# Kernel tuning notes

Measured on AMD Instinct MI355X. Metric: run time of the kernel, lower is better.

Reference implementation:

```python
import jax, jax.numpy as jnp
from jax import lax
import numpy as np

B, T, I, H, L, O = 256, 512, 1, 256, 4, 1


def setup_inputs() -> dict:
    key = jax.random.key(0)
    ks = jax.random.split(key, 4 * L + 3)
    s = 1.0 / np.sqrt(H)
    inp = {"x": jax.random.normal(ks[0], (B, T, I), dtype=jnp.float32)}
    for l in range(L):
        in_dim = I if l == 0 else H
        inp[f"W_ih{l}"] = jax.random.uniform(ks[1 + 4 * l], (4 * H, in_dim), minval=-s, maxval=s, dtype=jnp.float32)
        inp[f"W_hh{l}"] = jax.random.uniform(ks[2 + 4 * l], (4 * H, H), minval=-s, maxval=s, dtype=jnp.float32)
        inp[f"b_ih{l}"] = jax.random.uniform(ks[3 + 4 * l], (4 * H,), minval=-s, maxval=s, dtype=jnp.float32)
        inp[f"b_hh{l}"] = jax.random.uniform(ks[4 + 4 * l], (4 * H,), minval=-s, maxval=s, dtype=jnp.float32)
    inp["fc_W"] = jax.random.uniform(ks[-2], (O, H), minval=-s, maxval=s, dtype=jnp.float32)
    inp["fc_b"] = jax.random.uniform(ks[-1], (O,), minval=-s, maxval=s, dtype=jnp.float32)
    return inp


def _lstm_layer(x_seq, W_ih, W_hh, b_ih, b_hh):
    # x_seq: [B, T, in_dim] -> hidden sequence [B, T, H]
    b, t = x_seq.shape[0], x_seq.shape[1]
    h = W_hh.shape[1]
    # precompute input projections for all timesteps: [T, B, 4H]
    xg = jnp.einsum('bti,gi->tbg', x_seq, W_ih) + b_ih + b_hh

    def step(carry, xg_t):
        hp, cp = carry
        gates = xg_t + hp @ W_hh.T  # [B, 4H]
        i, f, g, o = jnp.split(gates, 4, axis=-1)  # PyTorch gate order: i,f,g,o
        i = jax.nn.sigmoid(i)
        f = jax.nn.sigmoid(f)
        g = jnp.tanh(g)
        o = jax.nn.sigmoid(o)
        c = f * cp + i * g
        hn = o * jnp.tanh(c)
        return (hn, c), hn

    h0 = jnp.zeros((b, h), x_seq.dtype)
    _, hs = lax.scan(step, (h0, h0), xg)
    return jnp.transpose(hs, (1, 0, 2))  # [B, T, H]


def reference(x, W_ih0, W_hh0, b_ih0, b_hh0, W_ih1, W_hh1, b_ih1, b_hh1,
              W_ih2, W_hh2, b_ih2, b_hh2, W_ih3, W_hh3, b_ih3, b_hh3, fc_W, fc_b):
    layers = [(W_ih0, W_hh0, b_ih0, b_hh0), (W_ih1, W_hh1, b_ih1, b_hh1),
              (W_ih2, W_hh2, b_ih2, b_hh2), (W_ih3, W_hh3, b_ih3, b_hh3)]
    out = x
    for Wi, Wh, bi, bh in layers:
        out = _lstm_layer(out, Wi, Wh, bi, bh)
    # final linear on last timestep hidden: [B, H] -> [B, O]
    return out[:, -1, :] @ fc_W.T + fc_b
```

## Files before the change

### kernel.cpp

```cpp
#include <hip/hip_runtime.h>
#include <stdint.h>

#define T_ 512
#define H_ 256
#define MB 32
#define NBUF 8
#define ISLOT 8192
#define NWG 256

typedef __attribute__((ext_vector_type(8))) short  short8;
typedef __attribute__((ext_vector_type(4))) float  floatx4;
typedef __attribute__((ext_vector_type(4))) unsigned int uint4v;
typedef unsigned long long ull;

struct Params {
  const float* x;
  const float* Wih[4]; const float* Whh[4]; const float* bih[4]; const float* bhh[4];
  const float* fcW; const float* fcb;
  int*   flags;
  int*   xcd;
  short* hring;
};

__device__ __forceinline__ short f2bf(float f){
  uint32_t u = __builtin_bit_cast(uint32_t, f);
  u += 0x7fffu + ((u >> 16) & 1u);
  return (short)(u >> 16);
}
__device__ __forceinline__ float bf2f(short s){
  uint32_t u = ((uint32_t)(uint16_t)s) << 16;
  return __builtin_bit_cast(float, u);
}
__device__ __forceinline__ float sigm(float v){ return 1.0f / (1.0f + __expf(-v)); }
__device__ __forceinline__ float tanh_(float v){
  float a = fabsf(v);
  float e = __expf(-2.0f * a);
  float r = (1.0f - e) / (1.0f + e);
  return v < 0.0f ? -r : r;
}

__device__ __forceinline__ void a_st32(unsigned* p, unsigned v){
  __hip_atomic_store(p, v, __ATOMIC_RELAXED, __HIP_MEMORY_SCOPE_AGENT);
}
__device__ __forceinline__ int a_ldi(const int* p){
  return __hip_atomic_load(p, __ATOMIC_RELAXED, __HIP_MEMORY_SCOPE_AGENT);
}
__device__ __forceinline__ void a_sti(int* p, int v){
  __hip_atomic_store(p, v, __ATOMIC_RELAXED, __HIP_MEMORY_SCOPE_AGENT);
}

__device__ __forceinline__ int ctr_poll(const int* p){
  int v; int z = 0;
  asm volatile("global_atomic_add %0, %1, %2, off sc0\n\t"
               "s_waitcnt vmcnt(0)"
               : "=v"(v) : "v"(p), "v"(z) : "memory");
  return v;
}
__device__ __forceinline__ void ctr_post(int* p){
  int one = 1;
  asm volatile("global_atomic_add %0, %1, off" :: "v"(p), "v"(one) : "memory");
}

template<bool SL> __device__ __forceinline__ void ld16t(uint4v& d, const void* p){
  if constexpr (SL) asm volatile("global_load_dwordx4 %0, %1, off sc0 sc1" : "=v"(d) : "v"(p));
  else              asm volatile("global_load_dwordx4 %0, %1, off sc0"     : "=v"(d) : "v"(p));
}
template<bool SL> __device__ __forceinline__ void st32t(unsigned* p, unsigned v){
  if constexpr (SL) a_st32(p, v);
  else asm volatile("global_store_dword %0, %1, off sc0" :: "v"(p), "v"(v) : "memory");
}
typedef __attribute__((address_space(1))) const void as1void;
typedef __attribute__((address_space(3))) void       as3void;
__device__ __forceinline__ void gld_lds16(const void* g, void* l){
  __builtin_amdgcn_global_load_lds((as1void*)g, (as3void*)l, 16, 0, 1);
}
__device__ __forceinline__ void inv_l1(){
  asm volatile("buffer_inv sc0" ::: "memory");
}

__device__ __forceinline__ void ldf32(float& d, const void* p){
  asm volatile("global_load_dword %0, %1, off" : "=v"(d) : "v"(p));
}
template<int N> __device__ __forceinline__ void waitvm(){
  if constexpr (N == 0) asm volatile("s_waitcnt vmcnt(0)" ::: "memory");
  else if constexpr (N == 1) asm volatile("s_waitcnt vmcnt(1)" ::: "memory");
  else                       asm volatile("s_waitcnt vmcnt(4)" ::: "memory");
}
__device__ __forceinline__ void bar_lds(){
  asm volatile("s_waitcnt lgkmcnt(0)" ::: "memory");
  __builtin_amdgcn_s_barrier();
}
__device__ __forceinline__ void bar_only(){
  __builtin_amdgcn_s_barrier();
}

#define MFMA(a,b,c) __builtin_amdgcn_mfma_f32_16x16x32_bf16((a),(b),(c),0,0,0)

__device__ __forceinline__ void wpoll(const int* p, int thr, bool& dead){
  if (dead) return;
  int guard = 0;
  for (;;){
    int v = a_ldi(p);
    if (__all((int)(v >= thr))) break;
    if (++guard > (1 << 16)) { dead = true; break; }
  }
}

__device__ __forceinline__ void cpoll(const int* self, const int* up, const int* down,
                                      int t, bool& dead){
  if (dead) return;
  const int lane = threadIdx.x & 63;
  const int* p = nullptr; int thr = 0;
  if (lane == 0)            { p = self; thr = t; }
  else if (lane == 1 && up) { p = up;   thr = t + 2; }
  else if (lane == 2 && down && ((t & 3) == 0)){ p = down; thr = t - 4; }
  if (thr > T_) thr = T_;
  thr <<= 3;
  int guard = 0;
  for (;;){
    int v = p ? ctr_poll(p) : 0x7fffffff;
    if (__all((int)(v >= thr))) break;
    __builtin_amdgcn_s_sleep(1);
    if (++guard > (1 << 14)) { dead = true; break; }
  }
}

template<bool L0, bool SL>
__device__ __forceinline__ void run_cell(const Params& p, int g, int l, int slice,
    short* a_frag, float (*g_lds)[MB][34], float (*bias_lds)[32],
    float (*wih0_lds)[32], float* x0_lds)
{
  constexpr int KBT = L0 ? 8 : 16;
  const int tid = threadIdx.x, lane = tid & 63, wave = tid >> 6;
  const int n15 = lane & 15, q4 = lane >> 4;

  int* fl_self = p.flags + (g * 4 + l) * 32;
  int* fl_up   = L0 ? fl_self : fl_self - 32;
  int* fl_down = (l < 3) ? fl_self + 32 : fl_self;
  short* hr_self = p.hring + (size_t)((g * 4 + l) * NBUF) * ISLOT;
  const short* hr_up = L0 ? (const short*)nullptr
                          : hr_self - (size_t)NBUF * ISLOT;

  int* ctr_self = fl_self;
  const int* ctr_up   = L0 ? (const int*)nullptr : fl_self - 32;
  const int* ctr_down = (l < 3) ? fl_self + 32 : (const int*)nullptr;

  if (tid < 128){
    int gt = tid >> 5, j = tid & 31;
    int gr = gt * 256 + slice * 32 + j;
    bias_lds[gt][j] = p.bih[l][gr] + p.bhh[l][gr];
    if (L0) wih0_lds[gt][j] = p.Wih[0][gr];
  }

  short8 wf0[KBT], wf1[KBT];
  const int g0 = wave * 256 + slice * 32 + n15;
  const int g1 = g0 + 16;
  #pragma unroll
  for (int kb = 0; kb < KBT; ++kb){
    const float* base; int kk;
    if (L0)          { base = p.Whh[0]; kk = kb * 32 + q4 * 8; }
    else if (kb < 8) { base = p.Wih[l]; kk = kb * 32 + q4 * 8; }
    else             { base = p.Whh[l]; kk = (kb - 8) * 32 + q4 * 8; }
    const float* p0 = base + (size_t)g0 * H_ + kk;
    const float* p1 = base + (size_t)g1 * H_ + kk;
    short8 a, b;
    #pragma unroll
    for (int i = 0; i < 8; ++i){ a[i] = f2bf(p0[i]); b[i] = f2bf(p1[i]); }
    wf0[kb] = a; wf1[kb] = b;
  }

  float c00 = 0.f, c01 = 0.f, c10 = 0.f, c11 = 0.f;
  const int r0 = (tid >> 4) * 2, r1 = r0 + 1;
  const int pc = (tid & 15) * 2;

  const int* pp; int dlt;
  if (lane < 8)      { pp = fl_self + lane; dlt = 0; }
  else if (lane < 16){ if (L0){ pp = fl_self; dlt = -1000000; }
                       else   { pp = fl_up + (lane - 8); dlt = 2; } }
  else if (lane < 24){ if (l < 3){ pp = fl_down + (lane - 16); dlt = -7; }
                       else      { pp = fl_self; dlt = -1000000; } }
  else               { pp = fl_self + (lane & 7); dlt = -1000000; }
  bool dead = false;

  uint4v* fragv = (uint4v*)a_frag;
  uint4v px[4];
  float xcur = 0.f;

  if (!L0){
    if constexpr (SL){
      wpoll(fl_up + (lane & 7), 1, dead);
    } else {
      if (wave == 0) cpoll(ctr_self, ctr_up, ctr_down, -1, dead);
      __syncthreads();
      inv_l1();
    }
    const char* s = (const char*)hr_up;
    #pragma unroll
    for (int k = 0; k < 4; ++k) ld16t<SL>(px[k], s + (size_t)(k * 256 + tid) * 16);
  } else if (wave == 0 && lane < MB){
    ldf32(xcur, &p.x[(size_t)(g * MB + lane) * T_]);
  }
  waitvm<0>();
  __syncthreads();

  for (int t = 0; t < T_; ++t){
    const bool havh = (t > 0);
    const bool pf = (t + 1 < T_);
    const int hbase = L0 ? 0 : 1024;
    uint4v hv[4];
    floatx4 acc[2][2][2] = {};

    if constexpr (SL){
      { int thr = t + dlt; if (thr > T_) thr = T_;
        wpoll(pp, thr, dead); }
      if (!L0){
        #pragma unroll
        for (int k = 0; k < 4; ++k) fragv[k * 256 + tid] = px[k];
      } else if (wave == 0 && lane < MB){
        x0_lds[lane] = xcur;
      }
      if (havh){
        const char* s = (const char*)(hr_self + (size_t)((t - 1) & 7) * ISLOT);
        #pragma unroll
        for (int k = 0; k < 4; ++k) ld16t<SL>(hv[k], s + (size_t)(k * 256 + tid) * 16);
      }
      if (!L0){
        if (pf){
          const char* s = (const char*)(hr_up + (size_t)((t + 1) & 7) * ISLOT);
          #pragma unroll
          for (int k = 0; k < 4; ++k) ld16t<SL>(px[k], s + (size_t)(k * 256 + tid) * 16);
        }
      } else if (wave == 0 && lane < MB && pf){
        ldf32(xcur, &p.x[(size_t)(g * MB + lane) * T_ + (t + 1)]);
      }
      bar_lds();
      if (!L0){
        #pragma unroll
        for (int kb = 0; kb < 8; ++kb){
          #pragma unroll
          for (int mt = 0; mt < 2; ++mt){
            short8 af = *(short8*)&a_frag[(kb * 2 + mt) * 512 + lane * 8];
            int pr = kb & 1;
            acc[mt][0][pr] = MFMA(af, wf0[kb], acc[mt][0][pr]);
            acc[mt][1][pr] = MFMA(af, wf1[kb], acc[mt][1][pr]);
          }
        }
      }
      if (!L0){ if (pf) waitvm<4>(); else waitvm<0>(); }
      else    { if (wave == 0 && pf) waitvm<1>(); else waitvm<0>(); }
      if (havh){
        #pragma unroll
        for (int k = 0; k < 4; ++k) fragv[hbase + k * 256 + tid] = hv[k];
      } else {
        uint4v z = {0, 0, 0, 0};
        #pragma unroll
        for (int k = 0; k < 4; ++k) fragv[hbase + k * 256 + tid] = z;
      }
      bar_lds();
    } else if constexpr (!L0){
      #pragma unroll
      for (int k = 0; k < 4; ++k) fragv[k * 256 + tid] = px[k];
      bar_lds();
      #pragma unroll
      for (int kb = 0; kb < 4; ++kb){
        #pragma unroll
        for (int mt = 0; mt < 2; ++mt){
          short8 af = *(short8*)&a_frag[(kb * 2 + mt) * 512 + lane * 8];
          int pr = kb & 1;
          acc[mt][0][pr] = MFMA(af, wf0[kb], acc[mt][0][pr]);
          acc[mt][1][pr] = MFMA(af, wf1[kb], acc[mt][1][pr]);
        }
      }
      if (wave == 0) cpoll(ctr_self, ctr_up, ctr_down, t, dead);
      bar_only();
      inv_l1();
      if (havh){
        const char* s = (const char*)(hr_self + (size_t)((t - 1) & 7) * ISLOT);
        #pragma unroll
        for (int k = 0; k < 4; ++k){
          const char* src = s + (size_t)(k * 256 + tid) * 16;
          gld_lds16(src, (void*)&fragv[hbase + k * 256 + (tid & ~63)]);
        }
      }
      if (pf){
        const char* s = (const char*)(hr_up + (size_t)((t + 1) & 7) * ISLOT);
        #pragma unroll
        for (int k = 0; k < 4; ++k) ld16t<SL>(px[k], s + (size_t)(k * 256 + tid) * 16);
      }
      #pragma unroll
      for (int kb = 4; kb < 8; ++kb){
        #pragma unroll
        for (int mt = 0; mt < 2; ++mt){
          short8 af = *(short8*)&a_frag[(kb * 2 + mt) * 512 + lane * 8];
          int pr = kb & 1;
          acc[mt][0][pr] = MFMA(af, wf0[kb], acc[mt][0][pr]);
          acc[mt][1][pr] = MFMA(af, wf1[kb], acc[mt][1][pr]);
        }
      }
      if (pf) waitvm<4>(); else waitvm<0>();
      if (!havh){
        uint4v z = {0, 0, 0, 0};
        #pragma unroll
        for (int k = 0; k < 4; ++k) fragv[hbase + k * 256 + tid] = z;
      }
      bar_lds();
    } else {
      if (wave == 0) cpoll(ctr_self, ctr_up, ctr_down, t, dead);
      if (wave == 0 && lane < MB) x0_lds[lane] = xcur;
      bar_lds();
      inv_l1();
      if (havh){
        const char* s = (const char*)(hr_self + (size_t)((t - 1) & 7) * ISLOT);
        #pragma unroll
        for (int k = 0; k < 4; ++k){
          const char* src = s + (size_t)(k * 256 + tid) * 16;
          gld_lds16(src, (void*)&fragv[hbase + k * 256 + (tid & ~63)]);
        }
      }
      if (wave == 0 && lane < MB && pf){
        ldf32(xcur, &p.x[(size_t)(g * MB + lane) * T_ + (t + 1)]);
      }
      if (wave == 0 && pf) waitvm<1>(); else waitvm<0>();
      if (!havh){
        uint4v z = {0, 0, 0, 0};
        #pragma unroll
        for (int k = 0; k < 4; ++k) fragv[hbase + k * 256 + tid] = z;
      }
      bar_lds();
    }

    #pragma unroll
    for (int kb = (L0 ? 0 : 8); kb < KBT; ++kb){
      #pragma unroll
      for (int mt = 0; mt < 2; ++mt){
        short8 af = *(short8*)&a_frag[(kb * 2 + mt) * 512 + lane * 8];
        int pr = kb & 1;
        acc[mt][0][pr] = MFMA(af, wf0[kb], acc[mt][0][pr]);
        acc[mt][1][pr] = MFMA(af, wf1[kb], acc[mt][1][pr]);
      }
    }
    #pragma unroll
    for (int mt = 0; mt < 2; ++mt){
      floatx4 s0 = acc[mt][0][0] + acc[mt][0][1];
      floatx4 s1 = acc[mt][1][0] + acc[mt][1][1];
      int mrow = mt * 16 + q4 * 4;
      #pragma unroll
      for (int r = 0; r < 4; ++r){
        g_lds[wave][mrow + r][n15]      = s0[r];
        g_lds[wave][mrow + r][16 + n15] = s1[r];
      }
    }
    bar_lds();

    {
      float xs0 = 0.f, xs1 = 0.f;
      if (L0){ xs0 = x0_lds[r0]; xs1 = x0_lds[r1]; }
      float2 bi = *(const float2*)&bias_lds[0][pc];
      float2 bf = *(const float2*)&bias_lds[1][pc];
      float2 bg = *(const float2*)&bias_lds[2][pc];
      float2 bo = *(const float2*)&bias_lds[3][pc];
      float2 wi = {0.f,0.f}, wf = {0.f,0.f}, wg = {0.f,0.f}, wo = {0.f,0.f};
      if (L0){
        wi = *(const float2*)&wih0_lds[0][pc];
        wf = *(const float2*)&wih0_lds[1][pc];
        wg = *(const float2*)&wih0_lds[2][pc];
        wo = *(const float2*)&wih0_lds[3][pc];
      }
      short* slot = hr_self + (size_t)(t & 7) * ISLOT;
      #pragma unroll
      for (int rr = 0; rr < 2; ++rr){
        const int row = rr ? r1 : r0;
        const float xs = rr ? xs1 : xs0;
        float2 vi = *(const float2*)&g_lds[0][row][pc];
        float2 vf = *(const float2*)&g_lds[1][row][pc];
        float2 vg = *(const float2*)&g_lds[2][row][pc];
        float2 vo = *(const float2*)&g_lds[3][row][pc];
        float gi0 = vi.x + bi.x, gi1 = vi.y + bi.y;
        float gf0 = vf.x + bf.x, gf1 = vf.y + bf.y;
        float gg0 = vg.x + bg.x, gg1 = vg.y + bg.y;
        float go0 = vo.x + bo.x, go1 = vo.y + bo.y;
        if (L0){
          gi0 += xs * wi.x; gi1 += xs * wi.y;
          gf0 += xs * wf.x; gf1 += xs * wf.y;
          gg0 += xs * wg.x; gg1 += xs * wg.y;
          go0 += xs * wo.x; go1 += xs * wo.y;
        }
        float i0 = sigm(gi0), i1 = sigm(gi1);
        float f0 = sigm(gf0), f1 = sigm(gf1);
        float gv0 = tanh_(gg0), gv1 = tanh_(gg1);
        float o0 = sigm(go0), o1 = sigm(go1);
        float& ca = rr ? c10 : c00;
        float& cb = rr ? c11 : c01;
        ca = f0 * ca + i0 * gv0;
        cb = f1 * cb + i1 * gv1;
        float h0 = o0 * tanh_(ca);
        float h1 = o1 * tanh_(cb);
        unsigned pk = (unsigned)(uint16_t)f2bf(h0) | ((unsigned)(uint16_t)f2bf(h1) << 16);
        unsigned off = (unsigned)((slice * 2 + (row >> 4)) * 512
                     + ((pc >> 3) * 16 + (row & 15)) * 8 + (pc & 7));
        st32t<SL>((unsigned*)(slot + off), pk);
      }
    }

    waitvm<0>();
    bar_only();
    if (tid == 0){
      if constexpr (SL) a_sti(fl_self + slice, t + 1);
      else              ctr_post(ctr_self);
    }
  }
}

__global__ __launch_bounds__(256, 1) void lstm_kernel(Params p){
  __shared__ short a_frag[32 * 512];
  __shared__ float g_lds[4][MB][34];
  __shared__ float bias_lds[4][32];
  __shared__ float wih0_lds[4][32];
  __shared__ float x0_lds[MB];
  __shared__ int   fsh;

  const int bid   = blockIdx.x;
  const int g     = bid & 7;
  const int l     = (bid >> 3) & 3;
  const int slice = bid >> 5;

  int xcc;
  asm volatile("s_getreg_b32 %0, hwreg(HW_REG_XCC_ID)" : "=s"(xcc));
  const int me = xcc + 1;
  if (threadIdx.x == 0) a_sti(&p.xcd[bid], me);
  int fast;
  {
    const int lane = threadIdx.x & 63;
    const int idx = lane & 31;
    const int* xp = p.xcd + (idx >> 2) * 32 + (idx & 3) * 8 + g;
    int v = 0, guard = 0; bool giveup = false;
    for (;;){
      v = a_ldi(xp);
      if (__all((int)(v != 0))) break;
      if (++guard > (1 << 22)) { giveup = true; break; }
    }
    fast = (!giveup && __all((int)(v == me))) ? 1 : 0;
  }
  if (threadIdx.x == 0) fsh = 1;
  __syncthreads();
  if (!fast) fsh = 0;
  __syncthreads();
  fast = fsh;

  if (l == 0){
    if (fast) run_cell<true , false>(p, g, 0, slice, a_frag, g_lds, bias_lds, wih0_lds, x0_lds);
    else      run_cell<true , true >(p, g, 0, slice, a_frag, g_lds, bias_lds, wih0_lds, x0_lds);
  } else {
    if (fast) run_cell<false, false>(p, g, l, slice, a_frag, g_lds, bias_lds, wih0_lds, x0_lds);
    else      run_cell<false, true >(p, g, l, slice, a_frag, g_lds, bias_lds, wih0_lds, x0_lds);
  }
}

__global__ void fc_kernel(const short* __restrict__ hring, const float* __restrict__ fcW,
                          const float* __restrict__ fcb, float* __restrict__ out){
  int b = blockIdx.x, lane = threadIdx.x;
  int g = b >> 5, m = b & 31;
  int mt = m >> 4, mm = m & 15;
  const short* base = hring + (size_t)((g * 4 + 3) * NBUF + ((T_ - 1) & 7)) * ISLOT;
  float s = 0.f;
  #pragma unroll
  for (int k = 0; k < 4; ++k){
    int d = lane + 64 * k;
    int kb = d >> 5, koff = d & 31;
    short hv = base[(kb * 2 + mt) * 512 + ((koff >> 3) * 16 + mm) * 8 + (koff & 7)];
    s += bf2f(hv) * fcW[d];
  }
  #pragma unroll
  for (int off = 32; off; off >>= 1) s += __shfl_down(s, off);
  if (lane == 0) out[b] = s + fcb[0];
}

extern "C" void kernel_launch(void* const* d_in, const int* in_sizes, int n_in,
                              void* d_out, int out_size, void* d_ws, size_t ws_size,
                              hipStream_t stream) {
  Params P;
  P.x = (const float*)d_in[0];
  for (int l = 0; l < 4; ++l){
    P.Wih[l] = (const float*)d_in[1 + 4*l];
    P.Whh[l] = (const float*)d_in[2 + 4*l];
    P.bih[l] = (const float*)d_in[3 + 4*l];
    P.bhh[l] = (const float*)d_in[4 + 4*l];
  }
  P.fcW = (const float*)d_in[17];
  P.fcb = (const float*)d_in[18];

  char* ws = (char*)d_ws;
  P.flags = (int*)ws;
  P.xcd   = (int*)(ws + 4096);
  P.hring = (short*)(ws + 16384);

  hipMemsetAsync(ws, 0, 8192, stream);
  hipLaunchKernelGGL(lstm_kernel, dim3(NWG), dim3(256), 0, stream, P);
  hipLaunchKernelGGL(fc_kernel, dim3(256), dim3(64), 0, stream,
                     P.hring, P.fcW, P.fcb, (float*)d_out);
}
```

Baseline: 1.536 ms.

## Post per-wave counter arrivals and drop trailing barrier in counter-sync LSTM path

Restructures the non-flag (counter) synchronisation path so every wave polls the counters and posts its own arrival, instead of wave 0 polling and tid 0 posting after a block barrier. The poll threshold is scaled by 32 instead of 8 to match the per-wave posts. Layer-0 input staging is double-buffered so the next x value is written during the current step. The point is to remove a block-wide barrier and serial poll from each recurrent step, at the cost of more atomic traffic on the counters and more polling lanes.

```diff
diff --git a/kernel.cpp b/kernel.cpp
--- a/kernel.cpp
+++ b/kernel.cpp
@@ -115,7 +115,7 @@
   else if (lane == 1 && up) { p = up;   thr = t + 2; }
   else if (lane == 2 && down && ((t & 3) == 0)){ p = down; thr = t - 4; }
   if (thr > T_) thr = T_;
-  thr <<= 3;
+  thr <<= 5;
   int guard = 0;
   for (;;){
     int v = p ? ctr_poll(p) : 0x7fffffff;
@@ -128,7 +128,7 @@
 template<bool L0, bool SL>
 __device__ __forceinline__ void run_cell(const Params& p, int g, int l, int slice,
     short* a_frag, float (*g_lds)[MB][34], float (*bias_lds)[32],
-    float (*wih0_lds)[32], float* x0_lds)
+    float (*wih0_lds)[32], float (*x0_lds)[MB])
 {
   constexpr int KBT = L0 ? 8 : 16;
   const int tid = threadIdx.x, lane = tid & 63, wave = tid >> 6;
@@ -185,39 +185,95 @@
   uint4v* fragv = (uint4v*)a_frag;
   uint4v px[4];
   float xcur = 0.f;
-
-  if (!L0){
-    if constexpr (SL){
+  const int hbase = L0 ? 0 : 1024;
+
+  auto pointwise = [&](int t){
+    float xs0 = 0.f, xs1 = 0.f;
+    if (L0){ xs0 = x0_lds[t & 1][r0]; xs1 = x0_lds[t & 1][r1]; }
+    float2 bi = *(const float2*)&bias_lds[0][pc];
+    float2 bf = *(const float2*)&bias_lds[1][pc];
+    float2 bg = *(const float2*)&bias_lds[2][pc];
+    float2 bo = *(const float2*)&bias_lds[3][pc];
+    float2 wi = {0.f,0.f}, wf = {0.f,0.f}, wg = {0.f,0.f}, wo = {0.f,0.f};
+    if (L0){
+      wi = *(const float2*)&wih0_lds[0][pc];
+      wf = *(const float2*)&wih0_lds[1][pc];
+      wg = *(const float2*)&wih0_lds[2][pc];
+      wo = *(const float2*)&wih0_lds[3][pc];
+    }
+    short* slot = hr_self + (size_t)(t & 7) * ISLOT;
+    #pragma unroll
+    for (int rr = 0; rr < 2; ++rr){
+      const int row = rr ? r1 : r0;
+      const float xs = rr ? xs1 : xs0;
+      float2 vi = *(const float2*)&g_lds[0][row][pc];
+      float2 vf = *(const float2*)&g_lds[1][row][pc];
+      float2 vg = *(const float2*)&g_lds[2][row][pc];
+      float2 vo = *(const float2*)&g_lds[3][row][pc];
+      float gi0 = vi.x + bi.x, gi1 = vi.y + bi.y;
+      float gf0 = vf.x + bf.x, gf1 = vf.y + bf.y;
+      float gg0 = vg.x + bg.x, gg1 = vg.y + bg.y;
+      float go0 = vo.x + bo.x, go1 = vo.y + bo.y;
+      if (L0){
+        gi0 += xs * wi.x; gi1 += xs * wi.y;
+        gf0 += xs * wf.x; gf1 += xs * wf.y;
+        gg0 += xs * wg.x; gg1 += xs * wg.y;
+        go0 += xs * wo.x; go1 += xs * wo.y;
+      }
+      float i0 = sigm(gi0), i1 = sigm(gi1);
+      float f0 = sigm(gf0), f1 = sigm(gf1);
+      float gv0 = tanh_(gg0), gv1 = tanh_(gg1);
+      float o0 = sigm(go0), o1 = sigm(go1);
+      float& ca = rr ? c10 : c00;
+      float& cb = rr ? c11 : c01;
+      ca = f0 * ca + i0 * gv0;
+      cb = f1 * cb + i1 * gv1;
+      float h0 = o0 * tanh_(ca);
+      float h1 = o1 * tanh_(cb);
+      unsigned pk = (unsigned)(uint16_t)f2bf(h0) | ((unsigned)(uint16_t)f2bf(h1) << 16);
+      unsigned off = (unsigned)((slice * 2 + (row >> 4)) * 512
+                   + ((pc >> 3) * 16 + (row & 15)) * 8 + (pc & 7));
+      st32t<SL>((unsigned*)(slot + off), pk);
+    }
+  };
+  auto gates_out = [&](floatx4 (&acc)[2][2][2]){
+    #pragma unroll
+    for (int mt = 0; mt < 2; ++mt){
+      floatx4 s0 = acc[mt][0][0] + acc[mt][0][1];
+      floatx4 s1 = acc[mt][1][0] + acc[mt][1][1];
+      int mrow = mt * 16 + q4 * 4;
+      #pragma unroll
+      for (int r = 0; r < 4; ++r){
+        g_lds[wave][mrow + r][n15]      = s0[r];
+        g_lds[wave][mrow + r][16 + n15] = s1[r];
+      }
+    }
+  };
+
+  if constexpr (SL){
+    if (!L0){
       wpoll(fl_up + (lane & 7), 1, dead);
-    } else {
-      if (wave == 0) cpoll(ctr_self, ctr_up, ctr_down, -1, dead);
-      __syncthreads();
-      inv_l1();
-    }
-    const char* s = (const char*)hr_up;
-    #pragma unroll
-    for (int k = 0; k < 4; ++k) ld16t<SL>(px[k], s + (size_t)(k * 256 + tid) * 16);
-  } else if (wave == 0 && lane < MB){
-    ldf32(xcur, &p.x[(size_t)(g * MB + lane) * T_]);
-  }
-  waitvm<0>();
-  __syncthreads();
-
-  for (int t = 0; t < T_; ++t){
-    const bool havh = (t > 0);
-    const bool pf = (t + 1 < T_);
-    const int hbase = L0 ? 0 : 1024;
-    uint4v hv[4];
-    floatx4 acc[2][2][2] = {};
-
-    if constexpr (SL){
+      const char* s = (const char*)hr_up;
+      #pragma unroll
+      for (int k = 0; k < 4; ++k) ld16t<SL>(px[k], s + (size_t)(k * 256 + tid) * 16);
+    } else if (wave == 0 && lane < MB){
+      ldf32(xcur, &p.x[(size_t)(g * MB + lane) * T_]);
+    }
+    waitvm<0>();
+    __syncthreads();
+
+    for (int t = 0; t < T_; ++t){
+      const bool havh = (t > 0);
+      const bool pf = (t + 1 < T_);
+      floatx4 acc[2][2][2] = {};
+      uint4v hv[4];
       { int thr = t + dlt; if (thr > T_) thr = T_;
         wpoll(pp, thr, dead); }
       if (!L0){
         #pragma unroll
         for (int k = 0; k < 4; ++k) fragv[k * 256 + tid] = px[k];
       } else if (wave == 0 && lane < MB){
-        x0_lds[lane] = xcur;
+        x0_lds[0][lane] = xcur;
       }
       if (havh){
         const char* s = (const char*)(hr_self + (size_t)((t - 1) & 7) * ISLOT);
@@ -257,12 +313,8 @@
         for (int k = 0; k < 4; ++k) fragv[hbase + k * 256 + tid] = z;
       }
       bar_lds();
-    } else if constexpr (!L0){
-      #pragma unroll
-      for (int k = 0; k < 4; ++k) fragv[k * 256 + tid] = px[k];
-      bar_lds();
-      #pragma unroll
-      for (int kb = 0; kb < 4; ++kb){
+      #pragma unroll
+      for (int kb = (L0 ? 0 : 8); kb < KBT; ++kb){
         #pragma unroll
         for (int mt = 0; mt < 2; ++mt){
           short8 af = *(short8*)&a_frag[(kb * 2 + mt) * 512 + lane * 8];
@@ -271,24 +323,79 @@
           acc[mt][1][pr] = MFMA(af, wf1[kb], acc[mt][1][pr]);
         }
       }
-      if (wave == 0) cpoll(ctr_self, ctr_up, ctr_down, t, dead);
+      gates_out(acc);
+      bar_lds();
+      {
+        float xs0 = 0.f, xs1 = 0.f;
+        if (L0){ xs0 = x0_lds[0][r0]; xs1 = x0_lds[0][r1]; }
+        float2 bi = *(const float2*)&bias_lds[0][pc];
+        float2 bf = *(const float2*)&bias_lds[1][pc];
+        float2 bg = *(const float2*)&bias_lds[2][pc];
+        float2 bo = *(const float2*)&bias_lds[3][pc];
+        float2 wi = {0.f,0.f}, wf = {0.f,0.f}, wg = {0.f,0.f}, wo = {0.f,0.f};
+        if (L0){
+          wi = *(const float2*)&wih0_lds[0][pc];
+          wf = *(const float2*)&wih0_lds[1][pc];
+          wg = *(const float2*)&wih0_lds[2][pc];
+          wo = *(const float2*)&wih0_lds[3][pc];
+        }
+        short* slot = hr_self + (size_t)(t & 7) * ISLOT;
+        #pragma unroll
+        for (int rr = 0; rr < 2; ++rr){
+          const int row = rr ? r1 : r0;
+          const float xs = rr ? xs1 : xs0;
+          float2 vi = *(const float2*)&g_lds[0][row][pc];
+          float2 vf = *(const float2*)&g_lds[1][row][pc];
+          float2 vg = *(const float2*)&g_lds[2][row][pc];
+          float2 vo = *(const float2*)&g_lds[3][row][pc];
+          float gi0 = vi.x + bi.x, gi1 = vi.y + bi.y;
+          float gf0 = vf.x + bf.x, gf1 = vf.y + bf.y;
+          float gg0 = vg.x + bg.x, gg1 = vg.y + bg.y;
+          float go0 = vo.x + bo.x, go1 = vo.y + bo.y;
+          if (L0){
+            gi0 += xs * wi.x; gi1 += xs * wi.y;
+            gf0 += xs * wf.x; gf1 += xs * wf.y;
+            gg0 += xs * wg.x; gg1 += xs * wg.y;
+            go0 += xs * wo.x; go1 += xs * wo.y;
+          }
+          float i0 = sigm(gi0), i1 = sigm(gi1);
+          float f0 = sigm(gf0), f1 = sigm(gf1);
+          float gv0 = tanh_(gg0), gv1 = tanh_(gg1);
+          float o0 = sigm(go0), o1 = sigm(go1);
+          float& ca = rr ? c10 : c00;
+          float& cb = rr ? c11 : c01;
+          ca = f0 * ca + i0 * gv0;
+          cb = f1 * cb + i1 * gv1;
+          float h0 = o0 * tanh_(ca);
+          float h1 = o1 * tanh_(cb);
+          unsigned pk = (unsigned)(uint16_t)f2bf(h0) | ((unsigned)(uint16_t)f2bf(h1) << 16);
+          unsigned off = (unsigned)((slice * 2 + (row >> 4)) * 512
+                       + ((pc >> 3) * 16 + (row & 15)) * 8 + (pc & 7));
+          st32t<SL>((unsigned*)(slot + off), pk);
+        }
+      }
+      waitvm<0>();
       bar_only();
-      inv_l1();
-      if (havh){
-        const char* s = (const char*)(hr_self + (size_t)((t - 1) & 7) * ISLOT);
-        #pragma unroll
-        for (int k = 0; k < 4; ++k){
-          const char* src = s + (size_t)(k * 256 + tid) * 16;
-          gld_lds16(src, (void*)&fragv[hbase + k * 256 + (tid & ~63)]);
-        }
-      }
-      if (pf){
-        const char* s = (const char*)(hr_up + (size_t)((t + 1) & 7) * ISLOT);
-        #pragma unroll
-        for (int k = 0; k < 4; ++k) ld16t<SL>(px[k], s + (size_t)(k * 256 + tid) * 16);
-      }
-      #pragma unroll
-      for (int kb = 4; kb < 8; ++kb){
+      if (tid == 0) a_sti(fl_self + slice, t + 1);
+    }
+  } else if constexpr (!L0){
+    if (wave == 0) cpoll(ctr_self, ctr_up, ctr_down, -1, dead);
+    __syncthreads();
+    inv_l1();
+    { const char* s = (const char*)hr_up;
+      #pragma unroll
+      for (int k = 0; k < 4; ++k) ld16t<false>(px[k], s + (size_t)(k * 256 + tid) * 16); }
+    waitvm<0>();
+    #pragma unroll
+    for (int k = 0; k < 4; ++k) fragv[k * 256 + tid] = px[k];
+    bar_lds();
+
+    for (int t = 0; t < T_; ++t){
+      const bool havh = (t > 0);
+      const bool pf = (t + 1 < T_);
+      floatx4 acc[2][2][2] = {};
+      #pragma unroll
+      for (int kb = 0; kb < 4; ++kb){
         #pragma unroll
         for (int mt = 0; mt < 2; ++mt){
           short8 af = *(short8*)&a_frag[(kb * 2 + mt) * 512 + lane * 8];
@@ -297,17 +404,7 @@
           acc[mt][1][pr] = MFMA(af, wf1[kb], acc[mt][1][pr]);
         }
       }
-      if (pf) waitvm<4>(); else waitvm<0>();
-      if (!havh){
-        uint4v z = {0, 0, 0, 0};
-        #pragma unroll
-        for (int k = 0; k < 4; ++k) fragv[hbase + k * 256 + tid] = z;
-      }
-      bar_lds();
-    } else {
-      if (wave == 0) cpoll(ctr_self, ctr_up, ctr_down, t, dead);
-      if (wave == 0 && lane < MB) x0_lds[lane] = xcur;
-      bar_lds();
+      cpoll(ctr_self, ctr_up, ctr_down, t, dead);
       inv_l1();
       if (havh){
         const char* s = (const char*)(hr_self + (size_t)((t - 1) & 7) * ISLOT);
@@ -317,96 +414,94 @@
           gld_lds16(src, (void*)&fragv[hbase + k * 256 + (tid & ~63)]);
         }
       }
+      if (pf){
+        const char* s = (const char*)(hr_up + (size_t)((t + 1) & 7) * ISLOT);
+        #pragma unroll
+        for (int k = 0; k < 4; ++k) ld16t<false>(px[k], s + (size_t)(k * 256 + tid) * 16);
+      }
+      #pragma unroll
+      for (int kb = 4; kb < 8; ++kb){
+        #pragma unroll
+        for (int mt = 0; mt < 2; ++mt){
+          short8 af = *(short8*)&a_frag[(kb * 2 + mt) * 512 + lane * 8];
+          int pr = kb & 1;
+          acc[mt][0][pr] = MFMA(af, wf0[kb], acc[mt][0][pr]);
+          acc[mt][1][pr] = MFMA(af, wf1[kb], acc[mt][1][pr]);
+        }
+      }
+      waitvm<0>();
+      if (!havh){
+        uint4v z = {0, 0, 0, 0};
+        #pragma unroll
+        for (int k = 0; k < 4; ++k) fragv[hbase + k * 256 + tid] = z;
+      }
+      bar_lds();
+      if (pf){
+        #pragma unroll
+        for (int k = 0; k < 4; ++k) fragv[k * 256 + tid] = px[k];
+      }
+      #pragma unroll
+      for (int kb = 8; kb < 16; ++kb){
+        #pragma unroll
+        for (int mt = 0; mt < 2; ++mt){
+          short8 af = *(short8*)&a_frag[(kb * 2 + mt) * 512 + lane * 8];
+          int pr = kb & 1;
+          acc[mt][0][pr] = MFMA(af, wf0[kb], acc[mt][0][pr]);
+          acc[mt][1][pr] = MFMA(af, wf1[kb], acc[mt][1][pr]);
+        }
+      }
+      gates_out(acc);
+      bar_lds();
+      pointwise(t);
+      waitvm<0>();
+      if (lane == 0) ctr_post(ctr_self);
+    }
+  } else {
+    if (wave == 0 && lane < MB) ldf32(xcur, &p.x[(size_t)(g * MB + lane) * T_]);
+    waitvm<0>();
+    if (wave == 0 && lane < MB) x0_lds[0][lane] = xcur;
+    bar_lds();
+
+    for (int t = 0; t < T_; ++t){
+      const bool havh = (t > 0);
+      const bool pf = (t + 1 < T_);
+      floatx4 acc[2][2][2] = {};
+      cpoll(ctr_self, (const int*)nullptr, ctr_down, t, dead);
+      inv_l1();
+      if (havh){
+        const char* s = (const char*)(hr_self + (size_t)((t - 1) & 7) * ISLOT);
+        #pragma unroll
+        for (int k = 0; k < 4; ++k){
+          const char* src = s + (size_t)(k * 256 + tid) * 16;
+          gld_lds16(src, (void*)&fragv[hbase + k * 256 + (tid & ~63)]);
+        }
+      }
       if (wave == 0 && lane < MB && pf){
         ldf32(xcur, &p.x[(size_t)(g * MB + lane) * T_ + (t + 1)]);
       }
-      if (wave == 0 && pf) waitvm<1>(); else waitvm<0>();
+      waitvm<0>();
       if (!havh){
         uint4v z = {0, 0, 0, 0};
         #pragma unroll
         for (int k = 0; k < 4; ++k) fragv[hbase + k * 256 + tid] = z;
       }
       bar_lds();
-    }
-
-    #pragma unroll
-    for (int kb = (L0 ? 0 : 8); kb < KBT; ++kb){
-      #pragma unroll
-      for (int mt = 0; mt < 2; ++mt){
-        short8 af = *(short8*)&a_frag[(kb * 2 + mt) * 512 + lane * 8];
-        int pr = kb & 1;
-        acc[mt][0][pr] = MFMA(af, wf0[kb], acc[mt][0][pr]);
-        acc[mt][1][pr] = MFMA(af, wf1[kb], acc[mt][1][pr]);
-      }
-    }
-    #pragma unroll
-    for (int mt = 0; mt < 2; ++mt){
-      floatx4 s0 = acc[mt][0][0] + acc[mt][0][1];
-      floatx4 s1 = acc[mt][1][0] + acc[mt][1][1];
-      int mrow = mt * 16 + q4 * 4;
-      #pragma unroll
-      for (int r = 0; r < 4; ++r){
-        g_lds[wave][mrow + r][n15]      = s0[r];
-        g_lds[wave][mrow + r][16 + n15] = s1[r];
-      }
-    }
-    bar_lds();
-
-    {
-      float xs0 = 0.f, xs1 = 0.f;
-      if (L0){ xs0 = x0_lds[r0]; xs1 = x0_lds[r1]; }
-      float2 bi = *(const float2*)&bias_lds[0][pc];
-      float2 bf = *(const float2*)&bias_lds[1][pc];
-      float2 bg = *(const float2*)&bias_lds[2][pc];
-      float2 bo = *(const float2*)&bias_lds[3][pc];
-      float2 wi = {0.f,0.f}, wf = {0.f,0.f}, wg = {0.f,0.f}, wo = {0.f,0.f};
-      if (L0){
-        wi = *(const float2*)&wih0_lds[0][pc];
-        wf = *(const float2*)&wih0_lds[1][pc];
-        wg = *(const float2*)&wih0_lds[2][pc];
-        wo = *(const float2*)&wih0_lds[3][pc];
-      }
-      short* slot = hr_self + (size_t)(t & 7) * ISLOT;
-      #pragma unroll
-      for (int rr = 0; rr < 2; ++rr){
-        const int row = rr ? r1 : r0;
-        const float xs = rr ? xs1 : xs0;
-        float2 vi = *(const float2*)&g_lds[0][row][pc];
-        float2 vf = *(const float2*)&g_lds[1][row][pc];
-        float2 vg = *(const float2*)&g_lds[2][row][pc];
-        float2 vo = *(const float2*)&g_lds[3][row][pc];
-        float gi0 = vi.x + bi.x, gi1 = vi.y + bi.y;
-        float gf0 = vf.x + bf.x, gf1 = vf.y + bf.y;
-        float gg0 = vg.x + bg.x, gg1 = vg.y + bg.y;
-        float go0 = vo.x + bo.x, go1 = vo.y + bo.y;
-        if (L0){
-          gi0 += xs * wi.x; gi1 += xs * wi.y;
-          gf0 += xs * wf.x; gf1 += xs * wf.y;
-          gg0 += xs * wg.x; gg1 += xs * wg.y;
-          go0 += xs * wo.x; go1 += xs * wo.y;
-        }
-        float i0 = sigm(gi0), i1 = sigm(gi1);
-        float f0 = sigm(gf0), f1 = sigm(gf1);
-        float gv0 = tanh_(gg0), gv1 = tanh_(gg1);
-        float o0 = sigm(go0), o1 = sigm(go1);
-        float& ca = rr ? c10 : c00;
-        float& cb = rr ? c11 : c01;
-        ca = f0 * ca + i0 * gv0;
-        cb = f1 * cb + i1 * gv1;
-        float h0 = o0 * tanh_(ca);
-        float h1 = o1 * tanh_(cb);
-        unsigned pk = (unsigned)(uint16_t)f2bf(h0) | ((unsigned)(uint16_t)f2bf(h1) << 16);
-        unsigned off = (unsigned)((slice * 2 + (row >> 4)) * 512
-                     + ((pc >> 3) * 16 + (row & 15)) * 8 + (pc & 7));
-        st32t<SL>((unsigned*)(slot + off), pk);
-      }
-    }
-
-    waitvm<0>();
-    bar_only();
-    if (tid == 0){
-      if constexpr (SL) a_sti(fl_self + slice, t + 1);
-      else              ctr_post(ctr_self);
+      if (wave == 0 && lane < MB && pf) x0_lds[(t + 1) & 1][lane] = xcur;
+      #pragma unroll
+      for (int kb = 0; kb < 8; ++kb){
+        #pragma unroll
+        for (int mt = 0; mt < 2; ++mt){
+          short8 af = *(short8*)&a_frag[(kb * 2 + mt) * 512 + lane * 8];
+          int pr = kb & 1;
+          acc[mt][0][pr] = MFMA(af, wf0[kb], acc[mt][0][pr]);
+          acc[mt][1][pr] = MFMA(af, wf1[kb], acc[mt][1][pr]);
+        }
+      }
+      gates_out(acc);
+      bar_lds();
+      pointwise(t);
+      waitvm<0>();
+      if (lane == 0) ctr_post(ctr_self);
     }
   }
 }
@@ -416,7 +511,7 @@
   __shared__ float g_lds[4][MB][34];
   __shared__ float bias_lds[4][32];
   __shared__ float wih0_lds[4][32];
-  __shared__ float x0_lds[MB];
+  __shared__ float x0_lds[2][MB];
   __shared__ int   fsh;
 
   const int bid   = blockIdx.x;
```

Measured after the change: 2.208 ms. +43.8%, slower.

## Split LSTM step loop per mode and overlap next-input LDS staging with recurrent MFMAs

Applied to the files above, without the earlier changes.

The shared time-step loop is split into three specialized loops, one each for the flag-polling mode, the upper layers with counters, and layer 0 with counters. The common gate-output and pointwise code moves into lambdas. In the counter-based upper-layer path, the next timestep's input fragment is now written to LDS inside the current step, after the recurrent barrier and during the second half of the MFMAs. This removes a separate barrier at the top of each step. Layer 0 no longer polls the upstream counter, and the wait before the barrier becomes a full drain, which may add latency.

```diff
diff --git a/kernel.cpp b/kernel.cpp
--- a/kernel.cpp
+++ b/kernel.cpp
@@ -185,32 +185,88 @@
   uint4v* fragv = (uint4v*)a_frag;
   uint4v px[4];
   float xcur = 0.f;
-
-  if (!L0){
-    if constexpr (SL){
+  const int hbase = L0 ? 0 : 1024;
+
+  auto gates_out = [&](floatx4 (&acc)[2][2][2]){
+    #pragma unroll
+    for (int mt = 0; mt < 2; ++mt){
+      floatx4 s0 = acc[mt][0][0] + acc[mt][0][1];
+      floatx4 s1 = acc[mt][1][0] + acc[mt][1][1];
+      int mrow = mt * 16 + q4 * 4;
+      #pragma unroll
+      for (int r = 0; r < 4; ++r){
+        g_lds[wave][mrow + r][n15]      = s0[r];
+        g_lds[wave][mrow + r][16 + n15] = s1[r];
+      }
+    }
+  };
+  auto pointwise = [&](int t){
+    float xs0 = 0.f, xs1 = 0.f;
+    if (L0){ xs0 = x0_lds[r0]; xs1 = x0_lds[r1]; }
+    float2 bi = *(const float2*)&bias_lds[0][pc];
+    float2 bf = *(const float2*)&bias_lds[1][pc];
+    float2 bg = *(const float2*)&bias_lds[2][pc];
+    float2 bo = *(const float2*)&bias_lds[3][pc];
+    float2 wi = {0.f,0.f}, wf = {0.f,0.f}, wg = {0.f,0.f}, wo = {0.f,0.f};
+    if (L0){
+      wi = *(const float2*)&wih0_lds[0][pc];
+      wf = *(const float2*)&wih0_lds[1][pc];
+      wg = *(const float2*)&wih0_lds[2][pc];
+      wo = *(const float2*)&wih0_lds[3][pc];
+    }
+    short* slot = hr_self + (size_t)(t & 7) * ISLOT;
+    #pragma unroll
+    for (int rr = 0; rr < 2; ++rr){
+      const int row = rr ? r1 : r0;
+      const float xs = rr ? xs1 : xs0;
+      float2 vi = *(const float2*)&g_lds[0][row][pc];
+      float2 vf = *(const float2*)&g_lds[1][row][pc];
+      float2 vg = *(const float2*)&g_lds[2][row][pc];
+      float2 vo = *(const float2*)&g_lds[3][row][pc];
+      float gi0 = vi.x + bi.x, gi1 = vi.y + bi.y;
+      float gf0 = vf.x + bf.x, gf1 = vf.y + bf.y;
+      float gg0 = vg.x + bg.x, gg1 = vg.y + bg.y;
+      float go0 = vo.x + bo.x, go1 = vo.y + bo.y;
+      if (L0){
+        gi0 += xs * wi.x; gi1 += xs * wi.y;
+        gf0 += xs * wf.x; gf1 += xs * wf.y;
+        gg0 += xs * wg.x; gg1 += xs * wg.y;
+        go0 += xs * wo.x; go1 += xs * wo.y;
+      }
+      float i0 = sigm(gi0), i1 = sigm(gi1);
+      float f0 = sigm(gf0), f1 = sigm(gf1);
+      float gv0 = tanh_(gg0), gv1 = tanh_(gg1);
+      float o0 = sigm(go0), o1 = sigm(go1);
+      float& ca = rr ? c10 : c00;
+      float& cb = rr ? c11 : c01;
+      ca = f0 * ca + i0 * gv0;
+      cb = f1 * cb + i1 * gv1;
+      float h0 = o0 * tanh_(ca);
+      float h1 = o1 * tanh_(cb);
+      unsigned pk = (unsigned)(uint16_t)f2bf(h0) | ((unsigned)(uint16_t)f2bf(h1) << 16);
+      unsigned off = (unsigned)((slice * 2 + (row >> 4)) * 512
+                   + ((pc >> 3) * 16 + (row & 15)) * 8 + (pc & 7));
+      st32t<SL>((unsigned*)(slot + off), pk);
+    }
+  };
+
+  if constexpr (SL){
+    if (!L0){
       wpoll(fl_up + (lane & 7), 1, dead);
-    } else {
-      if (wave == 0) cpoll(ctr_self, ctr_up, ctr_down, -1, dead);
-      __syncthreads();
-      inv_l1();
-    }
-    const char* s = (const char*)hr_up;
-    #pragma unroll
-    for (int k = 0; k < 4; ++k) ld16t<SL>(px[k], s + (size_t)(k * 256 + tid) * 16);
-  } else if (wave == 0 && lane < MB){
-    ldf32(xcur, &p.x[(size_t)(g * MB + lane) * T_]);
-  }
-  waitvm<0>();
-  __syncthreads();
-
-  for (int t = 0; t < T_; ++t){
-    const bool havh = (t > 0);
-    const bool pf = (t + 1 < T_);
-    const int hbase = L0 ? 0 : 1024;
-    uint4v hv[4];
-    floatx4 acc[2][2][2] = {};
-
-    if constexpr (SL){
+      const char* s = (const char*)hr_up;
+      #pragma unroll
+      for (int k = 0; k < 4; ++k) ld16t<SL>(px[k], s + (size_t)(k * 256 + tid) * 16);
+    } else if (wave == 0 && lane < MB){
+      ldf32(xcur, &p.x[(size_t)(g * MB + lane) * T_]);
+    }
+    waitvm<0>();
+    __syncthreads();
+
+    for (int t = 0; t < T_; ++t){
+      const bool havh = (t > 0);
+      const bool pf = (t + 1 < T_);
+      floatx4 acc[2][2][2] = {};
+      uint4v hv[4];
       { int thr = t + dlt; if (thr > T_) thr = T_;
         wpoll(pp, thr, dead); }
       if (!L0){
@@ -257,12 +313,8 @@
         for (int k = 0; k < 4; ++k) fragv[hbase + k * 256 + tid] = z;
       }
       bar_lds();
-    } else if constexpr (!L0){
-      #pragma unroll
-      for (int k = 0; k < 4; ++k) fragv[k * 256 + tid] = px[k];
-      bar_lds();
-      #pragma unroll
-      for (int kb = 0; kb < 4; ++kb){
+      #pragma unroll
+      for (int kb = (L0 ? 0 : 8); kb < KBT; ++kb){
         #pragma unroll
         for (int mt = 0; mt < 2; ++mt){
           short8 af = *(short8*)&a_frag[(kb * 2 + mt) * 512 + lane * 8];
@@ -271,6 +323,39 @@
           acc[mt][1][pr] = MFMA(af, wf1[kb], acc[mt][1][pr]);
         }
       }
+      gates_out(acc);
+      bar_lds();
+      pointwise(t);
+      waitvm<0>();
+      bar_only();
+      if (tid == 0) a_sti(fl_self + slice, t + 1);
+    }
+  } else if constexpr (!L0){
+    if (wave == 0) cpoll(ctr_self, ctr_up, ctr_down, -1, dead);
+    __syncthreads();
+    inv_l1();
+    { const char* s = (const char*)hr_up;
+      #pragma unroll
+      for (int k = 0; k < 4; ++k) ld16t<false>(px[k], s + (size_t)(k * 256 + tid) * 16); }
+    waitvm<0>();
+    #pragma unroll
+    for (int k = 0; k < 4; ++k) fragv[k * 256 + tid] = px[k];
+    bar_lds();
+
+    for (int t = 0; t < T_; ++t){
+      const bool havh = (t > 0);
+      const bool pf = (t + 1 < T_);
+      floatx4 acc[2][2][2] = {};
+      #pragma unroll
+      for (int kb = 0; kb < 4; ++kb){
+        #pragma unroll
+        for (int mt = 0; mt < 2; ++mt){
+          short8 af = *(short8*)&a_frag[(kb * 2 + mt) * 512 + lane * 8];
+          int pr = kb & 1;
+          acc[mt][0][pr] = MFMA(af, wf0[kb], acc[mt][0][pr]);
+          acc[mt][1][pr] = MFMA(af, wf1[kb], acc[mt][1][pr]);
+        }
+      }
       if (wave == 0) cpoll(ctr_self, ctr_up, ctr_down, t, dead);
       bar_only();
       inv_l1();
@@ -285,7 +370,7 @@
       if (pf){
         const char* s = (const char*)(hr_up + (size_t)((t + 1) & 7) * ISLOT);
         #pragma unroll
-        for (int k = 0; k < 4; ++k) ld16t<SL>(px[k], s + (size_t)(k * 256 + tid) * 16);
+        for (int k = 0; k < 4; ++k) ld16t<false>(px[k], s + (size_t)(k * 256 + tid) * 16);
       }
       #pragma unroll
       for (int kb = 4; kb < 8; ++kb){
@@ -297,15 +382,44 @@
           acc[mt][1][pr] = MFMA(af, wf1[kb], acc[mt][1][pr]);
         }
       }
-      if (pf) waitvm<4>(); else waitvm<0>();
+      waitvm<0>();
       if (!havh){
         uint4v z = {0, 0, 0, 0};
         #pragma unroll
         for (int k = 0; k < 4; ++k) fragv[hbase + k * 256 + tid] = z;
       }
       bar_lds();
-    } else {
-      if (wave == 0) cpoll(ctr_self, ctr_up, ctr_down, t, dead);
+      if (pf){
+        #pragma unroll
+        for (int k = 0; k < 4; ++k) fragv[k * 256 + tid] = px[k];
+      }
+      #pragma unroll
+      for (int kb = 8; kb < 16; ++kb){
+        #pragma unroll
+        for (int mt = 0; mt < 2; ++mt){
+          short8 af = *(short8*)&a_frag[(kb * 2 + mt) * 512 + lane * 8];
+          int pr = kb & 1;
+          acc[mt][0][pr] = MFMA(af, wf0[kb], acc[mt][0][pr]);
+          acc[mt][1][pr] = MFMA(af, wf1[kb], acc[mt][1][pr]);
+        }
+      }
+      gates_out(acc);
+      bar_lds();
+      pointwise(t);
+      waitvm<0>();
+      bar_only();
+      if (tid == 0) ctr_post(ctr_self);
+    }
+  } else {
+    if (wave == 0 && lane < MB) ldf32(xcur, &p.x[(size_t)(g * MB + lane) * T_]);
+    waitvm<0>();
+    __syncthreads();
+
+    for (int t = 0; t < T_; ++t){
+      const bool havh = (t > 0);
+      const bool pf = (t + 1 < T_);
+      floatx4 acc[2][2][2] = {};
+      if (wave == 0) cpoll(ctr_self, (const int*)nullptr, ctr_down, t, dead);
       if (wave == 0 && lane < MB) x0_lds[lane] = xcur;
       bar_lds();
       inv_l1();
@@ -327,86 +441,22 @@
         for (int k = 0; k < 4; ++k) fragv[hbase + k * 256 + tid] = z;
       }
       bar_lds();
-    }
-
-    #pragma unroll
-    for (int kb = (L0 ? 0 : 8); kb < KBT; ++kb){
-      #pragma unroll
-      for (int mt = 0; mt < 2; ++mt){
-        short8 af = *(short8*)&a_frag[(kb * 2 + mt) * 512 + lane * 8];
-        int pr = kb & 1;
-        acc[mt][0][pr] = MFMA(af, wf0[kb], acc[mt][0][pr]);
-        acc[mt][1][pr] = MFMA(af, wf1[kb], acc[mt][1][pr]);
-      }
-    }
-    #pragma unroll
-    for (int mt = 0; mt < 2; ++mt){
-      floatx4 s0 = acc[mt][0][0] + acc[mt][0][1];
-      floatx4 s1 = acc[mt][1][0] + acc[mt][1][1];
-      int mrow = mt * 16 + q4 * 4;
-      #pragma unroll
-      for (int r = 0; r < 4; ++r){
-        g_lds[wave][mrow + r][n15]      = s0[r];
-        g_lds[wave][mrow + r][16 + n15] = s1[r];
-      }
-    }
-    bar_lds();
-
-    {
-      float xs0 = 0.f, xs1 = 0.f;
-      if (L0){ xs0 = x0_lds[r0]; xs1 = x0_lds[r1]; }
-      float2 bi = *(const float2*)&bias_lds[0][pc];
-      float2 bf = *(const float2*)&bias_lds[1][pc];
-      float2 bg = *(const float2*)&bias_lds[2][pc];
-      float2 bo = *(const float2*)&bias_lds[3][pc];
-      float2 wi = {0.f,0.f}, wf = {0.f,0.f}, wg = {0.f,0.f}, wo = {0.f,0.f};
-      if (L0){
-        wi = *(const float2*)&wih0_lds[0][pc];
-        wf = *(const float2*)&wih0_lds[1][pc];
-        wg = *(const float2*)&wih0_lds[2][pc];
-        wo = *(const float2*)&wih0_lds[3][pc];
-      }
-      short* slot = hr_self + (size_t)(t & 7) * ISLOT;
-      #pragma unroll
-      for (int rr = 0; rr < 2; ++rr){
-        const int row = rr ? r1 : r0;
-        const float xs = rr ? xs1 : xs0;
-        float2 vi = *(const float2*)&g_lds[0][row][pc];
-        float2 vf = *(const float2*)&g_lds[1][row][pc];
-        float2 vg = *(const float2*)&g_lds[2][row][pc];
-        float2 vo = *(const float2*)&g_lds[3][row][pc];
-        float gi0 = vi.x + bi.x, gi1 = vi.y + bi.y;
-        float gf0 = vf.x + bf.x, gf1 = vf.y + bf.y;
-        float gg0 = vg.x + bg.x, gg1 = vg.y + bg.y;
-        float go0 = vo.x + bo.x, go1 = vo.y + bo.y;
-        if (L0){
-          gi0 += xs * wi.x; gi1 += xs * wi.y;
-          gf0 += xs * wf.x; gf1 += xs * wf.y;
-          gg0 += xs * wg.x; gg1 += xs * wg.y;
-          go0 += xs * wo.x; go1 += xs * wo.y;
-        }
-        float i0 = sigm(gi0), i1 = sigm(gi1);
-        float f0 = sigm(gf0), f1 = sigm(gf1);
-        float gv0 = tanh_(gg0), gv1 = tanh_(gg1);
-        float o0 = sigm(go0), o1 = sigm(go1);
-        float& ca = rr ? c10 : c00;
-        float& cb = rr ? c11 : c01;
-        ca = f0 * ca + i0 * gv0;
-        cb = f1 * cb + i1 * gv1;
-        float h0 = o0 * tanh_(ca);
-        float h1 = o1 * tanh_(cb);
-        unsigned pk = (unsigned)(uint16_t)f2bf(h0) | ((unsigned)(uint16_t)f2bf(h1) << 16);
-        unsigned off = (unsigned)((slice * 2 + (row >> 4)) * 512
-                     + ((pc >> 3) * 16 + (row & 15)) * 8 + (pc & 7));
-        st32t<SL>((unsigned*)(slot + off), pk);
-      }
-    }
-
-    waitvm<0>();
-    bar_only();
-    if (tid == 0){
-      if constexpr (SL) a_sti(fl_self + slice, t + 1);
-      else              ctr_post(ctr_self);
+      #pragma unroll
+      for (int kb = 0; kb < 8; ++kb){
+        #pragma unroll
+        for (int mt = 0; mt < 2; ++mt){
+          short8 af = *(short8*)&a_frag[(kb * 2 + mt) * 512 + lane * 8];
+          int pr = kb & 1;
+          acc[mt][0][pr] = MFMA(af, wf0[kb], acc[mt][0][pr]);
+          acc[mt][1][pr] = MFMA(af, wf1[kb], acc[mt][1][pr]);
+        }
+      }
+      gates_out(acc);
+      bar_lds();
+      pointwise(t);
+      waitvm<0>();
+      bar_only();
+      if (tid == 0) ctr_post(ctr_self);
     }
   }
 }
```

Result: no change. 1.546 ms (+0.7%).
